# Kernel tuning notes

Hardware: AMD Instinct MI355X
Metric: run time of the kernel (lower is better)

## Reference

```python
import jax, jax.numpy as jnp
import numpy as np
import math

T = 1024        # num tokens
HIDDEN = 2880
HD = 64         # head_dim
NH = 64         # attention heads
NKV = 8         # kv heads
SW = 128        # sliding window (layer_idx=0 -> even -> active)
QKV_DIM = HD * (NH + 2 * NKV)  # 5120


def _rope_cos_sin(num_tokens):
    # YaRN (NTK-by-parts) rotary tables; all constants from ModelConfig defaults.
    base = 150000.0; scaling = 32.0; init_ctx = 4096.0
    ntk_alpha = 1.0; ntk_beta = 32.0
    d_half = HD / 2
    freq = base ** (np.arange(0, HD, 2, dtype=np.float32) / HD)
    concentration = 0.1 * math.log(scaling) + 1.0
    low = d_half * math.log(init_ctx / (ntk_beta * 2 * math.pi)) / math.log(base)
    high = d_half * math.log(init_ctx / (ntk_alpha * 2 * math.pi)) / math.log(base)
    interpolation = 1.0 / (scaling * freq)
    extrapolation = 1.0 / freq
    ramp = (np.arange(int(d_half), dtype=np.float32) - low) / (high - low)
    m = 1.0 - np.clip(ramp, 0.0, 1.0)
    inv_freq = interpolation * (1.0 - m) + extrapolation * m
    t = np.arange(num_tokens, dtype=np.float32)
    freqs = t[:, None] * inv_freq[None, :]
    cos = (np.cos(freqs) * concentration).astype(np.float32)
    sin = (np.sin(freqs) * concentration).astype(np.float32)
    return jnp.asarray(cos), jnp.asarray(sin)  # [T, HD//2]


def _apply_rope(x, cos, sin):
    # x: [T, H, HD]; cos/sin: [T, 1, HD//2]
    half = x.shape[-1] // 2
    x1, x2 = x[..., :half], x[..., half:]
    return jnp.concatenate([x1 * cos - x2 * sin, x2 * cos + x1 * sin], axis=-1)


def setup_inputs() -> dict:
    key = jax.random.key(0)
    ks = jax.random.split(key, 7)
    return {
        "x": jax.random.normal(ks[0], (T, HIDDEN), jnp.float32),
        "norm_scale": jnp.ones((HIDDEN,), jnp.float32),
        "qkv_w": jax.random.normal(ks[1], (QKV_DIM, HIDDEN), jnp.float32) / math.sqrt(HIDDEN),
        "qkv_b": jax.random.normal(ks[2], (QKV_DIM,), jnp.float32) * 0.02,
        "out_w": jax.random.normal(ks[3], (HIDDEN, NH * HD), jnp.float32) / math.sqrt(NH * HD),
        "out_b": jax.random.normal(ks[4], (HIDDEN,), jnp.float32) * 0.02,
        "sinks": jax.random.normal(ks[5], (NH,), jnp.float32),
    }


def reference(x, norm_scale, qkv_w, qkv_b, out_w, out_b, sinks):
    # --- RMSNorm ---
    t = x * jax.lax.rsqrt(jnp.mean(x * x, axis=-1, keepdims=True) + 1e-5) * norm_scale
    # --- fused QKV projection ---
    qkv = t @ qkv_w.T + qkv_b                      # [T, 5120]
    q_end = NH * HD
    k_end = q_end + NKV * HD
    q = qkv[:, :q_end].reshape(T, NH, HD)
    k = qkv[:, q_end:k_end].reshape(T, NKV, HD)
    v = qkv[:, k_end:].reshape(T, NKV, HD)
    # --- RoPE (YaRN) ---
    cos, sin = _rope_cos_sin(T)
    cos = cos[:, None, :]; sin = sin[:, None, :]   # [T, 1, HD//2]
    q = _apply_rope(q, cos, sin)
    k = _apply_rope(k, cos, sin)
    # --- GQA expand ---
    groups = NH // NKV
    k_e = jnp.repeat(k, groups, axis=1)            # [T, NH, HD]
    v_e = jnp.repeat(v, groups, axis=1)
    # --- scores + causal & sliding-window mask ---
    sm_scale = 1.0 / math.sqrt(HD)
    QK = jnp.einsum('qhd,khd->hqk', q, k_e) * sm_scale  # [NH, T, T]
    qi = jnp.arange(T)
    ki = jnp.arange(T)
    mask = (qi[:, None] < ki[None, :]) | (qi[:, None] >= ki[None, :] + SW)
    QK = jnp.where(mask[None], -jnp.inf, QK)
    # --- learned per-head sink logit appended to the softmax ---
    sink_col = jnp.broadcast_to(sinks[:, None, None], (NH, T, 1))
    logits = jnp.concatenate([QK, sink_col], axis=-1)   # [NH, T, T+1]
    W = jax.nn.softmax(logits, axis=-1)[..., :-1]       # drop sink prob
    # --- weighted values + output projection ---
    attn = jnp.einsum('hqk,khd->qhd', W, v_e)            # [T, NH, HD]
    return attn.reshape(T, NH * HD) @ out_w.T + out_b    # [T, HIDDEN]
```

## Files before the change

kernel.cpp:

```cpp
#include <hip/hip_runtime.h>
#include <hip/hip_bf16.h>
#include <math.h>

#define T_TOK 1024
#define HIDDEN 2880
#define HD 64
#define NH 64
#define NKV 8
#define SW 128
#define QKV_DIM 5120
#define ATTN_DIM 4096
#define OW_NPAD 2944
#define ROPE_END 4608

typedef __attribute__((ext_vector_type(8))) short sv8;
typedef __attribute__((ext_vector_type(8))) _Float16 h8;
typedef __attribute__((ext_vector_type(4))) float f32x4;

__device__ __forceinline__ ushort f2bf(float f) {
    union { float f; unsigned u; } v; v.f = f;
    unsigned r = v.u + 0x7fffu + ((v.u >> 16) & 1u);
    return (ushort)(r >> 16);
}
__device__ __forceinline__ float bf2f(ushort h) {
    union { unsigned u; float f; } v; v.u = ((unsigned)h) << 16;
    return v.f;
}
__device__ __forceinline__ void gload16(const ushort* g, ushort* l) {
    __builtin_amdgcn_global_load_lds(
        (const __attribute__((address_space(1))) unsigned int*)g,
        (__attribute__((address_space(3))) unsigned int*)l, 16, 0, 0);
}

__global__ void rope_table_kernel(float* __restrict__ cosT, float* __restrict__ sinT) {
    int gid = blockIdx.x * 256 + threadIdx.x;
    int i = gid & 31;
    int t = gid >> 5;
    const double d_half = 32.0;
    double freq = pow(150000.0, (double)i / 32.0);
    double lowd  = d_half * log(4096.0 / (32.0 * 2.0 * M_PI)) / log(150000.0);
    double highd = d_half * log(4096.0 / (2.0 * M_PI)) / log(150000.0);
    double ramp = ((double)i - lowd) / (highd - lowd);
    ramp = fmin(fmax(ramp, 0.0), 1.0);
    double m = 1.0 - ramp;
    double inv_freq = (1.0 / (32.0 * freq)) * (1.0 - m) + (1.0 / freq) * m;
    float phase = (float)t * (float)inv_freq;
    double conc = 0.1 * log(32.0) + 1.0;
    cosT[gid] = (float)(cos((double)phase) * conc);
    sinT[gid] = (float)(sin((double)phase) * conc);
}

__global__ __launch_bounds__(256) void split_kernel(const float* __restrict__ X,
                                                    ushort* __restrict__ hi,
                                                    ushort* __restrict__ lo,
                                                    long n_src, long n_dst) {
    long i = ((long)blockIdx.x * 256 + threadIdx.x) * 4;
    if (i >= n_dst) return;
    float4 v = make_float4(0.f, 0.f, 0.f, 0.f);
    if (i < n_src) v = *(const float4*)(X + i);
    ushort4 h, l;
    h.x = f2bf(v.x); l.x = f2bf(v.x - bf2f(h.x));
    h.y = f2bf(v.y); l.y = f2bf(v.y - bf2f(h.y));
    h.z = f2bf(v.z); l.z = f2bf(v.z - bf2f(h.z));
    h.w = f2bf(v.w); l.w = f2bf(v.w - bf2f(h.w));
    *(ushort4*)(hi + i) = h;
    *(ushort4*)(lo + i) = l;
}

__global__ __launch_bounds__(256) void rmsnorm_kernel(const float* __restrict__ x,
                                                      const float* __restrict__ scale,
                                                      ushort* __restrict__ t_hi,
                                                      ushort* __restrict__ t_lo) {
    const int row = blockIdx.x;
    const int tid = threadIdx.x;
    const float4* xr = (const float4*)(x + (size_t)row * HIDDEN);
    float4 v[3];
    float ss = 0.f;
    int cnt = 0;
    for (int i = tid; i < HIDDEN / 4; i += 256) {
        float4 a = xr[i];
        v[cnt++] = a;
        ss += a.x * a.x + a.y * a.y + a.z * a.z + a.w * a.w;
    }
    #pragma unroll
    for (int off = 32; off; off >>= 1) ss += __shfl_xor(ss, off);
    __shared__ float red[4];
    if ((tid & 63) == 0) red[tid >> 6] = ss;
    __syncthreads();
    float total = red[0] + red[1] + red[2] + red[3];
    float inv = rsqrtf(total / (float)HIDDEN + 1e-5f);
    const float4* sc = (const float4*)scale;
    cnt = 0;
    for (int i = tid; i < HIDDEN / 4; i += 256) {
        float4 a = v[cnt++];
        float4 s4 = sc[i];
        float4 o;
        o.x = a.x * inv * s4.x; o.y = a.y * inv * s4.y;
        o.z = a.z * inv * s4.z; o.w = a.w * inv * s4.w;
        ushort4 h, l;
        h.x = f2bf(o.x); l.x = f2bf(o.x - bf2f(h.x));
        h.y = f2bf(o.y); l.y = f2bf(o.y - bf2f(h.y));
        h.z = f2bf(o.z); l.z = f2bf(o.z - bf2f(h.z));
        h.w = f2bf(o.w); l.w = f2bf(o.w - bf2f(h.w));
        *(ushort4*)(t_hi + (size_t)row * HIDDEN + i * 4) = h;
        *(ushort4*)(t_lo + (size_t)row * HIDDEN + i * 4) = l;
    }
}

template <bool ROPE>
__global__ __launch_bounds__(256, 2) void gemm_mfma_split(
    const ushort* __restrict__ Ahi, const ushort* __restrict__ Alo,
    const ushort* __restrict__ Bhi, const ushort* __restrict__ Blo,
    const float* __restrict__ bias, float* __restrict__ C,
    const float* __restrict__ cosT, const float* __restrict__ sinT,
    const int N, const int K)
{
    __shared__ __align__(16) ushort sAhi[64 * 64];
    __shared__ __align__(16) ushort sAlo[64 * 64];
    __shared__ __align__(16) ushort sBhi[128 * 64];
    __shared__ __align__(16) ushort sBlo[128 * 64];

    const int tid = threadIdx.x;
    const int cpx = gridDim.x >> 3;
    const int L = blockIdx.x;
    const int lin = (L & 7) * cpx + (L >> 3);
    const int m0 = (lin & 15) * 64;
    const int n0 = (lin >> 4) * 128;

    const int w = tid >> 6, lane = tid & 63;
    const int wr = (w >> 1) * 32, wc = (w & 1) * 64;
    const int fr = lane & 15, fq = lane >> 4;

    int offA[2], loffA[2], offB[4], loffB[4];
    #pragma unroll
    for (int q = 0; q < 2; ++q) {
        int c = tid + q * 256;
        int row = c >> 3, pc = c & 7;
        int gcol = (pc ^ (row & 7)) * 8;
        offA[q] = (m0 + row) * K + gcol;
        loffA[q] = c * 8;
    }
    #pragma unroll
    for (int q = 0; q < 4; ++q) {
        int c = tid + q * 256;
        int row = c >> 3, pc = c & 7;
        int gcol = (pc ^ (row & 7)) * 8;
        offB[q] = (n0 + row) * K + gcol;
        loffB[q] = c * 8;
    }

    f32x4 acc[2][4] = {};

    for (int k0 = 0; k0 < K; k0 += 64) {
        #pragma unroll
        for (int q = 0; q < 2; ++q) {
            gload16(Ahi + offA[q] + k0, sAhi + loffA[q]);
            gload16(Alo + offA[q] + k0, sAlo + loffA[q]);
        }
        #pragma unroll
        for (int q = 0; q < 4; ++q) {
            gload16(Bhi + offB[q] + k0, sBhi + loffB[q]);
            gload16(Blo + offB[q] + k0, sBlo + loffB[q]);
        }
        __syncthreads();
        #pragma unroll
        for (int ks = 0; ks < 2; ++ks) {
            sv8 ahi[2], alo[2], bhi[4], blo[4];
            const int cx = ((ks * 4 + fq) ^ (fr & 7)) * 8;
            #pragma unroll
            for (int i = 0; i < 2; ++i) {
                int ra = (wr + i * 16 + fr) * 64 + cx;
                ahi[i] = *(const sv8*)(sAhi + ra);
                alo[i] = *(const sv8*)(sAlo + ra);
            }
            #pragma unroll
            for (int j = 0; j < 4; ++j) {
                int rb = (wc + j * 16 + fr) * 64 + cx;
                bhi[j] = *(const sv8*)(sBhi + rb);
                blo[j] = *(const sv8*)(sBlo + rb);
            }
            #pragma unroll
            for (int i = 0; i < 2; ++i)
                #pragma unroll
                for (int j = 0; j < 4; ++j) {
                    acc[i][j] = __builtin_amdgcn_mfma_f32_16x16x32_bf16(ahi[i], bhi[j], acc[i][j], 0, 0, 0);
                    acc[i][j] = __builtin_amdgcn_mfma_f32_16x16x32_bf16(ahi[i], blo[j], acc[i][j], 0, 0, 0);
                    acc[i][j] = __builtin_amdgcn_mfma_f32_16x16x32_bf16(alo[i], bhi[j], acc[i][j], 0, 0, 0);
                }
        }
        __syncthreads();
    }

    if (ROPE) {
        const bool rope = (n0 + wc) < ROPE_END;
        #pragma unroll
        for (int j = 0; j < 2; ++j) {
            const int col1 = n0 + wc + j * 16 + fr;
            const int col2 = col1 + 32;
            const float b1 = bias[col1], b2 = bias[col2];
            const int d = j * 16 + fr;
            #pragma unroll
            for (int i = 0; i < 2; ++i) {
                #pragma unroll
                for (int r = 0; r < 4; ++r) {
                    int row = m0 + wr + i * 16 + fq * 4 + r;
                    float v1 = acc[i][j][r] + b1;
                    float v2 = acc[i][j + 2][r] + b2;
                    if (rope) {
                        float c = cosT[row * 32 + d], s = sinT[row * 32 + d];
                        float w1 = v1 * c - v2 * s;
                        float w2 = v2 * c + v1 * s;
                        v1 = w1; v2 = w2;
                    }
                    C[(size_t)row * N + col1] = v1;
                    C[(size_t)row * N + col2] = v2;
                }
            }
        }
    } else {
        #pragma unroll
        for (int j = 0; j < 4; ++j) {
            int col = n0 + wc + j * 16 + fr;
            if (col < N) {
                float bv = bias[col];
                #pragma unroll
                for (int i = 0; i < 2; ++i) {
                    int row = m0 + wr + i * 16 + fq * 4;
                    #pragma unroll
                    for (int r = 0; r < 4; ++r)
                        C[(size_t)(row + r) * N + col] = acc[i][j][r] + bv;
                }
            }
        }
    }
}

__global__ __launch_bounds__(256, 1) void attn_mfma_kernel(
    const float* __restrict__ qkv, const float* __restrict__ sinks,
    ushort* __restrict__ attn_hi, ushort* __restrict__ attn_lo)
{
    __shared__ __align__(16) char smem[122880];
    ushort*   Khi = (ushort*)smem;
    ushort*   Klo = (ushort*)(smem + 20480);
    _Float16* Wl  = (_Float16*)smem;
    _Float16* Vt  = (_Float16*)(smem + 98304);

    const int q0 = blockIdx.x * 32;
    const int g  = blockIdx.y;
    const int tid = threadIdx.x;
    const int w = tid >> 6, lane = tid & 63;
    const int fr = lane & 15, fq = lane >> 4;
    const int s0 = (q0 > 127) ? (q0 - 127) : 0;
    const int kmax = q0 + 32 - s0;

    for (int idx = tid; idx < 160 * 8; idx += 256) {
        int j = idx >> 3, c = idx & 7;
        float kv[8], vv[8];
        if (j < kmax) {
            const float* src = qkv + (size_t)(s0 + j) * QKV_DIM + ATTN_DIM + g * 64 + c * 8;
            *(float4*)&kv[0] = *(const float4*)src;
            *(float4*)&kv[4] = *(const float4*)(src + 4);
            const float* srcv = src + NKV * 64;
            *(float4*)&vv[0] = *(const float4*)srcv;
            *(float4*)&vv[4] = *(const float4*)(srcv + 4);
        } else {
            #pragma unroll
            for (int e = 0; e < 8; ++e) { kv[e] = 0.f; vv[e] = 0.f; }
        }
        sv8 hv, lv;
        #pragma unroll
        for (int e = 0; e < 8; ++e) {
            ushort h = f2bf(kv[e]);
            hv[e] = (short)h;
            lv[e] = (short)f2bf(kv[e] - bf2f(h));
        }
        int cs = c ^ (j & 7);
        *(sv8*)(Khi + j * 64 + cs * 8) = hv;
        *(sv8*)(Klo + j * 64 + cs * 8) = lv;
        int cj = j >> 3, jl = j & 7;
        #pragma unroll
        for (int e = 0; e < 8; ++e) {
            int d = c * 8 + e;
            int cp = (cj & 24) | ((cj & 7) ^ (d & 7));
            Vt[d * 192 + cp * 8 + jl] = (_Float16)vv[e];
        }
    }

    sv8 qhi[4][2], qlo[4][2];
    #pragma unroll
    for (int rf = 0; rf < 4; ++rf) {
        int hl = w * 2 + (rf >> 1);
        int qr = (rf & 1) * 16 + fr;
        const float* qrow = qkv + (size_t)(q0 + qr) * QKV_DIM + (g * 8 + hl) * 64;
        #pragma unroll
        for (int ks = 0; ks < 2; ++ks) {
            float v[8];
            *(float4*)&v[0] = *(const float4*)(qrow + ks * 32 + fq * 8);
            *(float4*)&v[4] = *(const float4*)(qrow + ks * 32 + fq * 8 + 4);
            #pragma unroll
            for (int e = 0; e < 8; ++e) {
                ushort h = f2bf(v[e]);
                qhi[rf][ks][e] = (short)h;
                qlo[rf][ks][e] = (short)f2bf(v[e] - bf2f(h));
            }
        }
    }

    __syncthreads();

    const int ncf = (kmax + 15) >> 4;
    f32x4 S[4][10] = {};
    #pragma unroll
    for (int ks = 0; ks < 2; ++ks) {
        #pragma unroll
        for (int cf = 0; cf < 10; ++cf) {
            if (cf < ncf) {
                int key = cf * 16 + fr;
                int cs = (ks * 4 + fq) ^ (key & 7);
                sv8 kh = *(const sv8*)(Khi + key * 64 + cs * 8);
                sv8 kl = *(const sv8*)(Klo + key * 64 + cs * 8);
                #pragma unroll
                for (int rf = 0; rf < 4; ++rf) {
                    S[rf][cf] = __builtin_amdgcn_mfma_f32_16x16x32_bf16(qhi[rf][ks], kh, S[rf][cf], 0, 0, 0);
                    S[rf][cf] = __builtin_amdgcn_mfma_f32_16x16x32_bf16(qlo[rf][ks], kh, S[rf][cf], 0, 0, 0);
                    S[rf][cf] = __builtin_amdgcn_mfma_f32_16x16x32_bf16(qhi[rf][ks], kl, S[rf][cf], 0, 0, 0);
                }
            }
        }
    }

    __syncthreads();

    float inv_s[4][4];
    #pragma unroll
    for (int rf = 0; rf < 4; ++rf) {
        float sink = sinks[g * 8 + w * 2 + (rf >> 1)];
        #pragma unroll
        for (int r = 0; r < 4; ++r) {
            int q = q0 + (rf & 1) * 16 + fq * 4 + r;
            float sv[10];
            float mx = sink;
            #pragma unroll
            for (int cf = 0; cf < 10; ++cf) {
                float v = S[rf][cf][r] * 0.125f;
                int kg = s0 + cf * 16 + fr;
                bool ok = (cf < ncf) && (kg <= q) && (kg + SW > q);
                v = ok ? v : -INFINITY;
                sv[cf] = v;
                mx = fmaxf(mx, v);
            }
            #pragma unroll
            for (int off = 1; off < 16; off <<= 1) mx = fmaxf(mx, __shfl_xor(mx, off));
            float sum = 0.f;
            #pragma unroll
            for (int cf = 0; cf < 10; ++cf) {
                float e = __expf(sv[cf] - mx);
                sv[cf] = e;
                sum += e;
            }
            #pragma unroll
            for (int off = 1; off < 16; off <<= 1) sum += __shfl_xor(sum, off);
            sum += __expf(sink - mx);
            inv_s[rf][r] = 1.f / sum;
            int row = w * 64 + rf * 16 + fq * 4 + r;
            #pragma unroll
            for (int cf = 0; cf < 10; ++cf) {
                if (cf < ncf) {
                    int key = cf * 16 + fr;
                    int cj = key >> 3;
                    int cp = (cj & 24) | ((cj & 7) ^ (row & 7));
                    Wl[row * 192 + cp * 8 + (key & 7)] = (_Float16)sv[cf];
                }
            }
        }
    }

    __syncthreads();

    const int nks = (kmax + 31) >> 5;
    f32x4 O[4][4] = {};
    #pragma unroll
    for (int ks = 0; ks < 5; ++ks) {
        if (ks < nks) {
            h8 a[4], b[4];
            int cj = ks * 4 + fq;
            #pragma unroll
            for (int rf = 0; rf < 4; ++rf) {
                int row = w * 64 + rf * 16 + fr;
                int cp = (cj & 24) | ((cj & 7) ^ (row & 7));
                a[rf] = *(const h8*)(Wl + row * 192 + cp * 8);
            }
            #pragma unroll
            for (int df = 0; df < 4; ++df) {
                int d = df * 16 + fr;
                int cp = (cj & 24) | ((cj & 7) ^ (d & 7));
                b[df] = *(const h8*)(Vt + d * 192 + cp * 8);
            }
            #pragma unroll
            for (int rf = 0; rf < 4; ++rf)
                #pragma unroll
                for (int df = 0; df < 4; ++df)
                    O[rf][df] = __builtin_amdgcn_mfma_f32_16x16x32_f16(a[rf], b[df], O[rf][df], 0, 0, 0);
        }
    }

    #pragma unroll
    for (int rf = 0; rf < 4; ++rf) {
        int H = g * 8 + w * 2 + (rf >> 1);
        #pragma unroll
        for (int df = 0; df < 4; ++df) {
            int d = df * 16 + fr;
            #pragma unroll
            for (int r = 0; r < 4; ++r) {
                int qr = (rf & 1) * 16 + fq * 4 + r;
                float v = O[rf][df][r] * inv_s[rf][r];
                size_t addr = (size_t)(q0 + qr) * ATTN_DIM + H * 64 + d;
                ushort h16 = f2bf(v);
                attn_hi[addr] = h16;
                attn_lo[addr] = f2bf(v - bf2f(h16));
            }
        }
    }
}

extern "C" void kernel_launch(void* const* d_in, const int* in_sizes, int n_in,
                              void* d_out, int out_size, void* d_ws, size_t ws_size,
                              hipStream_t stream) {
    const float* x          = (const float*)d_in[0];
    const float* norm_scale = (const float*)d_in[1];
    const float* qkv_w      = (const float*)d_in[2];
    const float* qkv_b      = (const float*)d_in[3];
    const float* out_w      = (const float*)d_in[4];
    const float* out_b      = (const float*)d_in[5];
    const float* sinks      = (const float*)d_in[6];
    float* out = (float*)d_out;

    char* p = (char*)d_ws;
    auto alloc = [&](size_t bytes) { char* r = p; p += (bytes + 255) & ~(size_t)255; return r; };
    const size_t W_ELEMS  = (size_t)QKV_DIM * HIDDEN;
    const size_t W_ELEMS2 = (size_t)OW_NPAD * ATTN_DIM;
    const size_t W_MAX = W_ELEMS > W_ELEMS2 ? W_ELEMS : W_ELEMS2;
    ushort* w_hi  = (ushort*)alloc(W_MAX * 2);
    ushort* w_lo  = (ushort*)alloc(W_MAX * 2);
    ushort* ab_hi  = (ushort*)alloc((size_t)T_TOK * ATTN_DIM * 2);
    ushort* ab_lo  = (ushort*)alloc((size_t)T_TOK * ATTN_DIM * 2);
    float*  qkv_buf = (float*)alloc((size_t)T_TOK * QKV_DIM * 4);
    float*  cosT   = (float*)alloc((size_t)T_TOK * 32 * 4);
    float*  sinT   = (float*)alloc((size_t)T_TOK * 32 * 4);

    rope_table_kernel<<<(T_TOK * 32) / 256, 256, 0, stream>>>(cosT, sinT);

    long n_qw = (long)QKV_DIM * HIDDEN;
    split_kernel<<<(int)(n_qw / 4 / 256), 256, 0, stream>>>(qkv_w, w_hi, w_lo, n_qw, n_qw);

    rmsnorm_kernel<<<T_TOK, 256, 0, stream>>>(x, norm_scale, ab_hi, ab_lo);

    gemm_mfma_split<true><<<(T_TOK / 64) * (QKV_DIM / 128), 256, 0, stream>>>(
        ab_hi, ab_lo, w_hi, w_lo, qkv_b, qkv_buf, cosT, sinT, QKV_DIM, HIDDEN);

    attn_mfma_kernel<<<dim3(T_TOK / 32, NKV), 256, 0, stream>>>(qkv_buf, sinks, ab_hi, ab_lo);

    long n_ow_src = (long)HIDDEN * ATTN_DIM;
    long n_ow_dst = (long)OW_NPAD * ATTN_DIM;
    split_kernel<<<(int)(n_ow_dst / 4 / 256), 256, 0, stream>>>(out_w, w_hi, w_lo, n_ow_src, n_ow_dst);

    gemm_mfma_split<false><<<(T_TOK / 64) * (OW_NPAD / 128), 256, 0, stream>>>(
        ab_hi, ab_lo, w_hi, w_lo, out_b, out, nullptr, nullptr, HIDDEN, ATTN_DIM);
}
```

Baseline: 399.2 us.

## Emit pre-split K and transposed fp16 V from QKV GEMM; halve attention query block

The QKV GEMM epilogue now writes K directly as bf16 hi/lo pairs in a per-KV-head layout and V as a transposed fp16 array, instead of fp32 into the shared qkv buffer. The attention kernel then loads K with direct global-to-LDS copies and V with vector loads, skipping the per-block fp32 conversion and transpose. The query block is cut from 32 to 16 rows, which shrinks LDS and registers so two blocks can share a CU and the grid doubles. In exchange each K/V window is reloaded by twice as many blocks, and the GEMM epilogue does scattered 2-byte stores.

```diff
diff --git a/kernel.cpp b/kernel.cpp
--- a/kernel.cpp
+++ b/kernel.cpp
@@ -12,6 +12,7 @@
 #define ATTN_DIM 4096
 #define OW_NPAD 2944
 #define ROPE_END 4608
+#define QBLK 16
 
 typedef __attribute__((ext_vector_type(8))) short sv8;
 typedef __attribute__((ext_vector_type(8))) _Float16 h8;
@@ -25,6 +26,9 @@
 __device__ __forceinline__ float bf2f(ushort h) {
     union { unsigned u; float f; } v; v.u = ((unsigned)h) << 16;
     return v.f;
+}
+__device__ __forceinline__ ushort f2h(float f) {
+    union { _Float16 h; ushort u; } v; v.h = (_Float16)f; return v.u;
 }
 __device__ __forceinline__ void gload16(const ushort* g, ushort* l) {
     __builtin_amdgcn_global_load_lds(
@@ -113,6 +117,7 @@
     const ushort* __restrict__ Bhi, const ushort* __restrict__ Blo,
     const float* __restrict__ bias, float* __restrict__ C,
     const float* __restrict__ cosT, const float* __restrict__ sinT,
+    ushort* __restrict__ khi, ushort* __restrict__ klo, ushort* __restrict__ vt,
     const int N, const int K)
 {
     __shared__ __align__(16) ushort sAhi[64 * 64];
@@ -192,28 +197,66 @@
     }
 
     if (ROPE) {
-        const bool rope = (n0 + wc) < ROPE_END;
-        #pragma unroll
-        for (int j = 0; j < 2; ++j) {
-            const int col1 = n0 + wc + j * 16 + fr;
-            const int col2 = col1 + 32;
-            const float b1 = bias[col1], b2 = bias[col2];
-            const int d = j * 16 + fr;
-            #pragma unroll
-            for (int i = 0; i < 2; ++i) {
-                #pragma unroll
-                for (int r = 0; r < 4; ++r) {
-                    int row = m0 + wr + i * 16 + fq * 4 + r;
-                    float v1 = acc[i][j][r] + b1;
-                    float v2 = acc[i][j + 2][r] + b2;
-                    if (rope) {
+        const int colbase = n0 + wc;
+        if (colbase < ATTN_DIM) {
+            #pragma unroll
+            for (int j = 0; j < 2; ++j) {
+                const int col1 = colbase + j * 16 + fr;
+                const float b1 = bias[col1], b2 = bias[col1 + 32];
+                const int d = j * 16 + fr;
+                #pragma unroll
+                for (int i = 0; i < 2; ++i) {
+                    #pragma unroll
+                    for (int r = 0; r < 4; ++r) {
+                        int row = m0 + wr + i * 16 + fq * 4 + r;
+                        float v1 = acc[i][j][r] + b1;
+                        float v2 = acc[i][j + 2][r] + b2;
                         float c = cosT[row * 32 + d], s = sinT[row * 32 + d];
                         float w1 = v1 * c - v2 * s;
                         float w2 = v2 * c + v1 * s;
-                        v1 = w1; v2 = w2;
+                        C[(size_t)row * N + col1] = w1;
+                        C[(size_t)row * N + col1 + 32] = w2;
                     }
-                    C[(size_t)row * N + col1] = v1;
-                    C[(size_t)row * N + col2] = v2;
+                }
+            }
+        } else if (colbase < ROPE_END) {
+            const int gk = (colbase - ATTN_DIM) >> 6;
+            #pragma unroll
+            for (int j = 0; j < 2; ++j) {
+                const int d1 = j * 16 + fr;
+                const float b1 = bias[colbase + d1], b2 = bias[colbase + d1 + 32];
+                #pragma unroll
+                for (int i = 0; i < 2; ++i) {
+                    #pragma unroll
+                    for (int r = 0; r < 4; ++r) {
+                        int row = m0 + wr + i * 16 + fq * 4 + r;
+                        float v1 = acc[i][j][r] + b1;
+                        float v2 = acc[i][j + 2][r] + b2;
+                        float c = cosT[row * 32 + d1], s = sinT[row * 32 + d1];
+                        float w1 = v1 * c - v2 * s;
+                        float w2 = v2 * c + v1 * s;
+                        size_t base = ((size_t)(gk << 10) + row) << 6;
+                        ushort h1 = f2bf(w1), h2 = f2bf(w2);
+                        khi[base + d1] = h1;       klo[base + d1] = f2bf(w1 - bf2f(h1));
+                        khi[base + d1 + 32] = h2;  klo[base + d1 + 32] = f2bf(w2 - bf2f(h2));
+                    }
+                }
+            }
+        } else {
+            const int cb = colbase - ROPE_END;
+            #pragma unroll
+            for (int j = 0; j < 4; ++j) {
+                const int col = cb + j * 16 + fr;
+                const float bv = bias[colbase + j * 16 + fr];
+                #pragma unroll
+                for (int i = 0; i < 2; ++i) {
+                    int row = m0 + wr + i * 16 + fq * 4;
+                    ushort4 st;
+                    st.x = f2h(acc[i][j][0] + bv);
+                    st.y = f2h(acc[i][j][1] + bv);
+                    st.z = f2h(acc[i][j][2] + bv);
+                    st.w = f2h(acc[i][j][3] + bv);
+                    *(ushort4*)(vt + ((size_t)col << 10) + row) = st;
                 }
             }
         }
@@ -235,63 +278,51 @@
     }
 }
 
-__global__ __launch_bounds__(256, 1) void attn_mfma_kernel(
-    const float* __restrict__ qkv, const float* __restrict__ sinks,
+__global__ __launch_bounds__(256, 2) void attn_mfma_kernel(
+    const float* __restrict__ qkv, const ushort* __restrict__ khi,
+    const ushort* __restrict__ klo, const ushort* __restrict__ vt,
+    const float* __restrict__ sinks,
     ushort* __restrict__ attn_hi, ushort* __restrict__ attn_lo)
 {
-    __shared__ __align__(16) char smem[122880];
+    __shared__ __align__(16) char smem[73728];
     ushort*   Khi = (ushort*)smem;
-    ushort*   Klo = (ushort*)(smem + 20480);
+    ushort*   Klo = (ushort*)(smem + 18432);
     _Float16* Wl  = (_Float16*)smem;
-    _Float16* Vt  = (_Float16*)(smem + 98304);
-
-    const int q0 = blockIdx.x * 32;
+    _Float16* Vt  = (_Float16*)(smem + 49152);
+
+    const int q0 = blockIdx.x * QBLK;
     const int g  = blockIdx.y;
     const int tid = threadIdx.x;
     const int w = tid >> 6, lane = tid & 63;
     const int fr = lane & 15, fq = lane >> 4;
     const int s0 = (q0 > 127) ? (q0 - 127) : 0;
-    const int kmax = q0 + 32 - s0;
-
-    for (int idx = tid; idx < 160 * 8; idx += 256) {
-        int j = idx >> 3, c = idx & 7;
-        float kv[8], vv[8];
-        if (j < kmax) {
-            const float* src = qkv + (size_t)(s0 + j) * QKV_DIM + ATTN_DIM + g * 64 + c * 8;
-            *(float4*)&kv[0] = *(const float4*)src;
-            *(float4*)&kv[4] = *(const float4*)(src + 4);
-            const float* srcv = src + NKV * 64;
-            *(float4*)&vv[0] = *(const float4*)srcv;
-            *(float4*)&vv[4] = *(const float4*)(srcv + 4);
-        } else {
-            #pragma unroll
-            for (int e = 0; e < 8; ++e) { kv[e] = 0.f; vv[e] = 0.f; }
-        }
-        sv8 hv, lv;
-        #pragma unroll
-        for (int e = 0; e < 8; ++e) {
-            ushort h = f2bf(kv[e]);
-            hv[e] = (short)h;
-            lv[e] = (short)f2bf(kv[e] - bf2f(h));
-        }
-        int cs = c ^ (j & 7);
-        *(sv8*)(Khi + j * 64 + cs * 8) = hv;
-        *(sv8*)(Klo + j * 64 + cs * 8) = lv;
-        int cj = j >> 3, jl = j & 7;
-        #pragma unroll
-        for (int e = 0; e < 8; ++e) {
-            int d = c * 8 + e;
-            int cp = (cj & 24) | ((cj & 7) ^ (d & 7));
-            Vt[d * 192 + cp * 8 + jl] = (_Float16)vv[e];
-        }
-    }
-
-    sv8 qhi[4][2], qlo[4][2];
-    #pragma unroll
-    for (int rf = 0; rf < 4; ++rf) {
-        int hl = w * 2 + (rf >> 1);
-        int qr = (rf & 1) * 16 + fr;
-        const float* qrow = qkv + (size_t)(q0 + qr) * QKV_DIM + (g * 8 + hl) * 64;
+    const int s0a = s0 & ~7;
+    const int kmax = q0 + QBLK - s0a;
+    const int ncf = kmax >> 4;
+    const int nks = (kmax + 31) >> 5;
+    const int kzend = nks << 5;
+
+    for (int idx = tid; idx < 144 * 8; idx += 256) {
+        if ((idx >> 3) < kmax) {
+            int j = idx >> 3, pc = idx & 7;
+            int src = (((g << 10) + s0a + j) << 6) + ((pc ^ (j & 7)) << 3);
+            gload16(khi + src, Khi + idx * 8);
+            gload16(klo + src, Klo + idx * 8);
+        }
+    }
+    for (int idx = tid; idx < 64 * 20; idx += 256) {
+        int d = idx / 20, cj = idx % 20;
+        int4 vdat = make_int4(0, 0, 0, 0);
+        if ((cj << 3) < kmax)
+            vdat = *(const int4*)(vt + (((size_t)(g << 6) + d) << 10) + s0a + (cj << 3));
+        int cp = (cj & 24) | ((cj & 7) ^ (d & 7));
+        *(int4*)(Vt + d * 192 + cp * 8) = vdat;
+    }
+
+    sv8 qhi[2][2], qlo[2][2];
+    #pragma unroll
+    for (int rf = 0; rf < 2; ++rf) {
+        const float* qrow = qkv + (size_t)(q0 + fr) * QKV_DIM + (g * 8 + w * 2 + rf) * 64;
         #pragma unroll
         for (int ks = 0; ks < 2; ++ks) {
             float v[8];
@@ -308,19 +339,18 @@
 
     __syncthreads();
 
-    const int ncf = (kmax + 15) >> 4;
-    f32x4 S[4][10] = {};
+    f32x4 S[2][9] = {};
     #pragma unroll
     for (int ks = 0; ks < 2; ++ks) {
         #pragma unroll
-        for (int cf = 0; cf < 10; ++cf) {
+        for (int cf = 0; cf < 9; ++cf) {
             if (cf < ncf) {
                 int key = cf * 16 + fr;
-                int cs = (ks * 4 + fq) ^ (key & 7);
-                sv8 kh = *(const sv8*)(Khi + key * 64 + cs * 8);
-                sv8 kl = *(const sv8*)(Klo + key * 64 + cs * 8);
-                #pragma unroll
-                for (int rf = 0; rf < 4; ++rf) {
+                int cs = ((ks * 4 + fq) ^ (key & 7)) * 8;
+                sv8 kh = *(const sv8*)(Khi + key * 64 + cs);
+                sv8 kl = *(const sv8*)(Klo + key * 64 + cs);
+                #pragma unroll
+                for (int rf = 0; rf < 2; ++rf) {
                     S[rf][cf] = __builtin_amdgcn_mfma_f32_16x16x32_bf16(qhi[rf][ks], kh, S[rf][cf], 0, 0, 0);
                     S[rf][cf] = __builtin_amdgcn_mfma_f32_16x16x32_bf16(qlo[rf][ks], kh, S[rf][cf], 0, 0, 0);
                     S[rf][cf] = __builtin_amdgcn_mfma_f32_16x16x32_bf16(qhi[rf][ks], kl, S[rf][cf], 0, 0, 0);
@@ -331,19 +361,19 @@
 
     __syncthreads();
 
-    float inv_s[4][4];
-    #pragma unroll
-    for (int rf = 0; rf < 4; ++rf) {
-        float sink = sinks[g * 8 + w * 2 + (rf >> 1)];
+    float inv_s[2][4];
+    #pragma unroll
+    for (int rf = 0; rf < 2; ++rf) {
+        float sink = sinks[g * 8 + w * 2 + rf];
         #pragma unroll
         for (int r = 0; r < 4; ++r) {
-            int q = q0 + (rf & 1) * 16 + fq * 4 + r;
-            float sv[10];
+            int q = q0 + fq * 4 + r;
+            float sv[10] = {};
             float mx = sink;
             #pragma unroll
-            for (int cf = 0; cf < 10; ++cf) {
+            for (int cf = 0; cf < 9; ++cf) {
                 float v = S[rf][cf][r] * 0.125f;
-                int kg = s0 + cf * 16 + fr;
+                int kg = s0a + cf * 16 + fr;
                 bool ok = (cf < ncf) && (kg <= q) && (kg + SW > q);
                 v = ok ? v : -INFINITY;
                 sv[cf] = v;
@@ -353,8 +383,8 @@
             for (int off = 1; off < 16; off <<= 1) mx = fmaxf(mx, __shfl_xor(mx, off));
             float sum = 0.f;
             #pragma unroll
-            for (int cf = 0; cf < 10; ++cf) {
-                float e = __expf(sv[cf] - mx);
+            for (int cf = 0; cf < 9; ++cf) {
+                float e = (cf < ncf) ? __expf(sv[cf] - mx) : 0.f;
                 sv[cf] = e;
                 sum += e;
             }
@@ -362,11 +392,11 @@
             for (int off = 1; off < 16; off <<= 1) sum += __shfl_xor(sum, off);
             sum += __expf(sink - mx);
             inv_s[rf][r] = 1.f / sum;
-            int row = w * 64 + rf * 16 + fq * 4 + r;
+            int row = w * 32 + rf * 16 + fq * 4 + r;
             #pragma unroll
             for (int cf = 0; cf < 10; ++cf) {
-                if (cf < ncf) {
-                    int key = cf * 16 + fr;
+                int key = cf * 16 + fr;
+                if (key < kzend) {
                     int cj = key >> 3;
                     int cp = (cj & 24) | ((cj & 7) ^ (row & 7));
                     Wl[row * 192 + cp * 8 + (key & 7)] = (_Float16)sv[cf];
@@ -377,16 +407,15 @@
 
     __syncthreads();
 
-    const int nks = (kmax + 31) >> 5;
-    f32x4 O[4][4] = {};
+    f32x4 O[2][4] = {};
     #pragma unroll
     for (int ks = 0; ks < 5; ++ks) {
         if (ks < nks) {
-            h8 a[4], b[4];
+            h8 a[2], b[4];
             int cj = ks * 4 + fq;
             #pragma unroll
-            for (int rf = 0; rf < 4; ++rf) {
-                int row = w * 64 + rf * 16 + fr;
+            for (int rf = 0; rf < 2; ++rf) {
+                int row = w * 32 + rf * 16 + fr;
                 int cp = (cj & 24) | ((cj & 7) ^ (row & 7));
                 a[rf] = *(const h8*)(Wl + row * 192 + cp * 8);
             }
@@ -397,7 +426,7 @@
                 b[df] = *(const h8*)(Vt + d * 192 + cp * 8);
             }
             #pragma unroll
-            for (int rf = 0; rf < 4; ++rf)
+            for (int rf = 0; rf < 2; ++rf)
                 #pragma unroll
                 for (int df = 0; df < 4; ++df)
                     O[rf][df] = __builtin_amdgcn_mfma_f32_16x16x32_f16(a[rf], b[df], O[rf][df], 0, 0, 0);
@@ -405,16 +434,15 @@
     }
 
     #pragma unroll
-    for (int rf = 0; rf < 4; ++rf) {
-        int H = g * 8 + w * 2 + (rf >> 1);
+    for (int rf = 0; rf < 2; ++rf) {
+        int H = g * 8 + w * 2 + rf;
         #pragma unroll
         for (int df = 0; df < 4; ++df) {
             int d = df * 16 + fr;
             #pragma unroll
             for (int r = 0; r < 4; ++r) {
-                int qr = (rf & 1) * 16 + fq * 4 + r;
                 float v = O[rf][df][r] * inv_s[rf][r];
-                size_t addr = (size_t)(q0 + qr) * ATTN_DIM + H * 64 + d;
+                size_t addr = (size_t)(q0 + fq * 4 + r) * ATTN_DIM + H * 64 + d;
                 ushort h16 = f2bf(v);
                 attn_hi[addr] = h16;
                 attn_lo[addr] = f2bf(v - bf2f(h16));
@@ -445,8 +473,11 @@
     ushort* ab_hi  = (ushort*)alloc((size_t)T_TOK * ATTN_DIM * 2);
     ushort* ab_lo  = (ushort*)alloc((size_t)T_TOK * ATTN_DIM * 2);
     float*  qkv_buf = (float*)alloc((size_t)T_TOK * QKV_DIM * 4);
-    float*  cosT   = (float*)alloc((size_t)T_TOK * 32 * 4);
-    float*  sinT   = (float*)alloc((size_t)T_TOK * 32 * 4);
+    ushort* khi = (ushort*)alloc((size_t)NKV * T_TOK * HD * 2);
+    ushort* klo = (ushort*)alloc((size_t)NKV * T_TOK * HD * 2);
+    ushort* vt  = (ushort*)alloc((size_t)NKV * HD * T_TOK * 2);
+    float*  cosT = (float*)alloc((size_t)T_TOK * 32 * 4);
+    float*  sinT = (float*)alloc((size_t)T_TOK * 32 * 4);
 
     rope_table_kernel<<<(T_TOK * 32) / 256, 256, 0, stream>>>(cosT, sinT);
 
@@ -456,14 +487,17 @@
     rmsnorm_kernel<<<T_TOK, 256, 0, stream>>>(x, norm_scale, ab_hi, ab_lo);
 
     gemm_mfma_split<true><<<(T_TOK / 64) * (QKV_DIM / 128), 256, 0, stream>>>(
-        ab_hi, ab_lo, w_hi, w_lo, qkv_b, qkv_buf, cosT, sinT, QKV_DIM, HIDDEN);
-
-    attn_mfma_kernel<<<dim3(T_TOK / 32, NKV), 256, 0, stream>>>(qkv_buf, sinks, ab_hi, ab_lo);
+        ab_hi, ab_lo, w_hi, w_lo, qkv_b, qkv_buf, cosT, sinT, khi, klo, vt,
+        QKV_DIM, HIDDEN);
+
+    attn_mfma_kernel<<<dim3(T_TOK / QBLK, NKV), 256, 0, stream>>>(
+        qkv_buf, khi, klo, vt, sinks, ab_hi, ab_lo);
 
     long n_ow_src = (long)HIDDEN * ATTN_DIM;
     long n_ow_dst = (long)OW_NPAD * ATTN_DIM;
     split_kernel<<<(int)(n_ow_dst / 4 / 256), 256, 0, stream>>>(out_w, w_hi, w_lo, n_ow_src, n_ow_dst);
 
     gemm_mfma_split<false><<<(T_TOK / 64) * (OW_NPAD / 128), 256, 0, stream>>>(
-        ab_hi, ab_lo, w_hi, w_lo, out_b, out, nullptr, nullptr, HIDDEN, ATTN_DIM);
-}
+        ab_hi, ab_lo, w_hi, w_lo, out_b, out, nullptr, nullptr,
+        nullptr, nullptr, nullptr, HIDDEN, ATTN_DIM);
+}
```

New measurement: 390.3 us. 2.2% less time.
